# Performance work log

Hardware: AMD Instinct MI355X
Metric: run time of the kernel (lower is better)

The kernel has to match this reference:

```python
import jax, jax.numpy as jnp
import numpy as np

D_MODEL = 96
N_HEAD = 3
HEAD_DIM = D_MODEL // N_HEAD  # 32
D_FF = 2048
WIDTH = 65
HALF_W = (WIDTH - 1) // 2  # 32
EPS = 1e-5


def layer_norm(x, g, b):
    mu = jnp.mean(x, axis=-1, keepdims=True)
    var = jnp.mean(jnp.square(x - mu), axis=-1, keepdims=True)
    return (x - mu) * jax.lax.rsqrt(var + EPS) * g + b


def setup_inputs() -> dict:
    key = jax.random.key(0)
    ks = jax.random.split(key, 8)
    B, T = 8, 2048
    s = 0.05
    return {
        "x": jax.random.normal(ks[0], (B, D_MODEL, T), dtype=jnp.float32),
        "w_qkv": jax.random.normal(ks[1], (3 * D_MODEL, D_MODEL), dtype=jnp.float32) * s,
        "b_qkv": jnp.zeros((3 * D_MODEL,), dtype=jnp.float32),
        "w_out": jax.random.normal(ks[2], (D_MODEL, D_MODEL), dtype=jnp.float32) * s,
        "b_out": jnp.zeros((D_MODEL,), dtype=jnp.float32),
        "ln1_g": jnp.ones((D_MODEL,), dtype=jnp.float32),
        "ln1_b": jnp.zeros((D_MODEL,), dtype=jnp.float32),
        "w_ff1": jax.random.normal(ks[3], (D_FF, D_MODEL), dtype=jnp.float32) * s,
        "b_ff1": jnp.zeros((D_FF,), dtype=jnp.float32),
        "w_ff2": jax.random.normal(ks[4], (D_MODEL, D_FF), dtype=jnp.float32) * s,
        "b_ff2": jnp.zeros((D_MODEL,), dtype=jnp.float32),
        "ln2_g": jnp.ones((D_MODEL,), dtype=jnp.float32),
        "ln2_b": jnp.zeros((D_MODEL,), dtype=jnp.float32),
        "lnf_g": jnp.ones((D_MODEL,), dtype=jnp.float32),
        "lnf_b": jnp.zeros((D_MODEL,), dtype=jnp.float32),
    }


def reference(x, w_qkv, b_qkv, w_out, b_out, ln1_g, ln1_b, w_ff1, b_ff1,
              w_ff2, b_ff2, ln2_g, ln2_b, lnf_g, lnf_b):
    # x: (B, C, T) -> (B, T, C)
    h = jnp.transpose(x, (0, 2, 1))
    B, T, C = h.shape

    # --- multi-head self-attention with banded mask ---
    qkv = h @ w_qkv.T + b_qkv                      # (B, T, 3C)
    q, k, v = jnp.split(qkv, 3, axis=-1)
    q = q.reshape(B, T, N_HEAD, HEAD_DIM)
    k = k.reshape(B, T, N_HEAD, HEAD_DIM)
    v = v.reshape(B, T, N_HEAD, HEAD_DIM)

    scale = 1.0 / jnp.sqrt(jnp.float32(HEAD_DIM))
    scores = jnp.einsum("bthd,bshd->bhts", q, k) * scale  # (B, H, T, T)

    idx = jnp.arange(T)
    band = jnp.abs(idx[:, None] - idx[None, :]) <= HALF_W  # |i-j| <= half width
    scores = jnp.where(band[None, None], scores, jnp.float32(-jnp.inf))

    attn = jax.nn.softmax(scores, axis=-1)
    ctx = jnp.einsum("bhts,bshd->bthd", attn, v).reshape(B, T, C)
    attn_out = ctx @ w_out.T + b_out

    # --- post-norm encoder layer (dropout inactive / eval mode) ---
    h = layer_norm(h + attn_out, ln1_g, ln1_b)
    ff = jax.nn.relu(h @ w_ff1.T + b_ff1) @ w_ff2.T + b_ff2
    h = layer_norm(h + ff, ln2_g, ln2_b)

    # extra layernorm applied when width is not None
    h = layer_norm(h, lnf_g, lnf_b)

    # (B, T, C) -> (B, C, T)
    return jnp.transpose(h, (0, 2, 1))
```

## Files before the change

kernel.cpp:

```cpp
#include <hip/hip_runtime.h>
#include <hip/hip_bf16.h>

#define B 8
#define T 2048
#define C 96
#define NH 3
#define HD 32
#define FFD 2048
#define HALF_W 32
#define BT (B*T)

typedef __hip_bfloat16 bf16;
typedef __attribute__((ext_vector_type(8))) short short8;
typedef __attribute__((ext_vector_type(4))) short short4v;
typedef __attribute__((ext_vector_type(16))) float floatx16;

__device__ __forceinline__ short f2bs(float v){
    __hip_bfloat16 h = __float2bfloat16(v);
    return *reinterpret_cast<short*>(&h);
}
__device__ __forceinline__ float bs2f(short s){
    unsigned u = ((unsigned)(unsigned short)s) << 16;
    return __uint_as_float(u);
}
__device__ __forceinline__ int imin(int a, int b){ return a < b ? a : b; }
__device__ __forceinline__ int imax(int a, int b){ return a > b ? a : b; }
__device__ __forceinline__ short8 ld_b64x2(const short* p){
    short4v a = *(const short4v*)p;
    short4v b = *(const short4v*)(p + 4);
    short8 v;
    v[0]=a[0]; v[1]=a[1]; v[2]=a[2]; v[3]=a[3];
    v[4]=b[0]; v[5]=b[1]; v[6]=b[2]; v[7]=b[3];
    return v;
}
__device__ __forceinline__ int4 exch_pair(int a0,int a1,int b0,int b1,int hq){
    int ra0=__shfl_xor(a0,32), ra1=__shfl_xor(a1,32);
    int rb0=__shfl_xor(b0,32), rb1=__shfl_xor(b1,32);
    int4 s;
    s.x = hq ? rb0 : a0;
    s.y = hq ? rb1 : a1;
    s.z = hq ? b0  : ra0;
    s.w = hq ? b1  : ra1;
    return s;
}

__global__ void cvtw_kernel(const float* __restrict__ wq, const float* __restrict__ wo,
                            const float* __restrict__ w1, const float* __restrict__ w2,
                            bf16* __restrict__ dst){
    int i = blockIdx.x*256 + threadIdx.x;
    if(i < 27648){
        int e = i&7, lane = (i>>3)&63, r = i>>9;
        int ks = r%6, ot = r/6;
        int o = ot*32 + (lane&31);
        int k = ks*16 + (lane>>5)*8 + e;
        dst[i] = __float2bfloat16(wq[o*96 + k]);
    } else if(i < 36864){
        int j = i - 27648;
        int e = j&7, lane = (j>>3)&63, r = j>>9;
        int ks = r%6, ct = r/6;
        int c = ct*32 + (lane&31);
        int k = ks*16 + (lane>>5)*8 + e;
        dst[i] = __float2bfloat16(wo[c*96 + k]);
    } else if(i < 233472){
        int j = i - 36864;
        int e = j&7, lane = (j>>3)&63, r = j>>9;
        int ks = r%6; r /= 6;
        int w = r%4, jt = r/4;
        int row = jt*128 + w*32 + (lane&31);
        int k = ks*16 + (lane>>5)*8 + e;
        dst[i] = __float2bfloat16(w1[row*96 + k]);
    } else if(i < 430080){
        int j = i - 233472;
        int e = j&7, lane = (j>>3)&63, r = j>>9;
        int ct = r%3; r /= 3;
        int g = r%2; r /= 2;
        int w = r%4, jt = r/4;
        int c = ct*32 + (lane&31);
        int k = jt*128 + w*32 + g*16 + (lane>>5)*8 + e;
        dst[i] = __float2bfloat16(w2[c*FFD + k]);
    }
}

__global__ __launch_bounds__(256) void qkv_kernel(
    const float* __restrict__ x, const bf16* __restrict__ wqs,
    const float* __restrict__ bias, bf16* __restrict__ qswz,
    bf16* __restrict__ kswz, bf16* __restrict__ vbuf){
    __shared__ float xs[96*36];
    int b  = blockIdx.x >> 6;
    int tt = blockIdx.x & 63;
    int t0 = tt * 32;
    for(int e = threadIdx.x; e < 96*8; e += 256){
        int c = e >> 3, t4 = e & 7;
        *(float4*)(xs + c*36 + t4*4) =
            *(const float4*)(x + (size_t)b*C*T + (size_t)c*T + t0 + t4*4);
    }
    __syncthreads();
    const int w = threadIdx.x >> 6, lane = threadIdx.x & 63;
    const int lm = lane & 31, hq = lane >> 5;
    short8 bfr[6];
    #pragma unroll
    for(int ks = 0; ks < 6; ++ks){
        short8 v;
        #pragma unroll
        for(int i = 0; i < 8; ++i)
            v[i] = f2bs(xs[(ks*16 + hq*8 + i)*36 + lm]);
        bfr[ks] = v;
    }
    int nacc = (w == 0) ? 3 : 2;
    int ots[3] = {w, w+4, 8};
    floatx16 acc[3];
    #pragma unroll
    for(int i = 0; i < 3; ++i)
        #pragma unroll
        for(int r = 0; r < 16; ++r) acc[i][r] = 0.f;
    #pragma unroll
    for(int i = 0; i < 3; ++i){
        if(i < nacc){
            #pragma unroll
            for(int ks = 0; ks < 6; ++ks){
                short8 af = *(const short8*)((const short*)wqs
                              + (size_t)(ots[i]*6 + ks)*512 + lane*8);
                acc[i] = __builtin_amdgcn_mfma_f32_32x32x16_bf16(af, bfr[ks], acc[i], 0,0,0);
            }
        }
    }
    #pragma unroll
    for(int i = 0; i < 3; ++i){
        if(i < nacc){
            int ot = ots[i];
            int pkq[4][2];
            #pragma unroll
            for(int q = 0; q < 4; ++q){
                float4 bv = *(const float4*)(bias + ot*32 + 8*q + 4*hq);
                short4v t;
                t[0] = f2bs(acc[i][4*q+0] + bv.x);
                t[1] = f2bs(acc[i][4*q+1] + bv.y);
                t[2] = f2bs(acc[i][4*q+2] + bv.z);
                t[3] = f2bs(acc[i][4*q+3] + bv.w);
                int2 u = *(int2*)&t;
                pkq[q][0] = u.x; pkq[q][1] = u.y;
            }
            if(ot < 6){
                int type = ot/3, hh = ot%3;
                short* base = (short*)(type == 0 ? qswz : kswz)
                            + ((size_t)(b*NH + hh)*64 + tt)*1024 + lane*8;
                #pragma unroll
                for(int g = 0; g < 2; ++g){
                    int a0 = pkq[2*g][0],   a1 = pkq[2*g][1];
                    int b0 = pkq[2*g+1][0], b1v = pkq[2*g+1][1];
                    int ra0 = __shfl_xor(a0, 32),  ra1 = __shfl_xor(a1, 32);
                    int rb0 = __shfl_xor(b0, 32),  rb1 = __shfl_xor(b1v, 32);
                    int4 sfi;
                    sfi.x = hq ? rb0 : a0;
                    sfi.y = hq ? rb1 : a1;
                    sfi.z = hq ? b0  : ra0;
                    sfi.w = hq ? b1v : ra1;
                    *(int4*)(base + g*512) = sfi;
                }
            } else {
                int hh = ot - 6;
                short* rowp = (short*)vbuf + ((size_t)(b*NH + hh)*T + t0 + lm)*32;
                #pragma unroll
                for(int q = 0; q < 4; ++q){
                    int2 u; u.x = pkq[q][0]; u.y = pkq[q][1];
                    *(int2*)(rowp + 8*q + 4*hq) = u;
                }
            }
        }
    }
}

__global__ __launch_bounds__(192) void attn_op_kernel(
    const bf16* __restrict__ qswz, const bf16* __restrict__ kswz,
    const bf16* __restrict__ vbuf, const bf16* __restrict__ wos,
    const float* __restrict__ bias, const float* __restrict__ x,
    const float* __restrict__ g1, const float* __restrict__ bb1,
    bf16* __restrict__ h1b){
    __shared__ __align__(16) short VtS[3*3200];
    __shared__ __align__(16) short PtS[3][3200];
    __shared__ float LsS[3][32];
    __shared__ __align__(16) short ctxS[32*100];
    __shared__ float red1[2][3][32];
    const int tid = threadIdx.x;
    const int w = tid / 64, lane = tid & 63;
    const int lm = lane & 31, hq = lane >> 5;
    int b  = blockIdx.x >> 6;
    int tt = blockIdx.x & 63;
    int t0 = tt * 32;

    short8 wof[6];
    #pragma unroll
    for(int ks = 0; ks < 6; ++ks)
        wof[ks] = *(const short8*)((const short*)wos + (size_t)(w*6 + ks)*512 + lane*8);

    for(int e = tid; e < 576; e += 192){
        int hh = e / 192, rem = e % 192;
        int kp = rem >> 2, d8 = rem & 3;
        const short* vb = (const short*)vbuf + (size_t)(b*NH + hh)*T*32;
        int sa = imin(imax(t0 - 32 + 2*kp, 0), T-1);
        int sb = imin(imax(t0 - 32 + 2*kp + 1, 0), T-1);
        short8 va = *(const short8*)(vb + (size_t)sa*32 + d8*8);
        short8 v2 = *(const short8*)(vb + (size_t)sb*32 + d8*8);
        #pragma unroll
        for(int j = 0; j < 8; ++j){
            int val = (int)(unsigned short)va[j] | ((int)(unsigned short)v2[j] << 16);
            *(int*)(VtS + hh*3200 + (d8*8 + j)*100 + 2*kp) = val;
        }
    }
    const short* qsw = (const short*)qswz + ((size_t)(b*NH + w)*64 + tt)*1024 + lane*8;
    short8 qf0 = *(const short8*)(qsw);
    short8 qf1 = *(const short8*)(qsw + 512);
    floatx16 S[3];
    #pragma unroll
    for(int sub = 0; sub < 3; ++sub){
        int kt = imin(imax(tt - 1 + sub, 0), 63);
        const short* ksw = (const short*)kswz + ((size_t)(b*NH + w)*64 + kt)*1024 + lane*8;
        short8 kf0 = *(const short8*)(ksw);
        short8 kf1 = *(const short8*)(ksw + 512);
        floatx16 z;
        #pragma unroll
        for(int r = 0; r < 16; ++r) z[r] = 0.f;
        z = __builtin_amdgcn_mfma_f32_32x32x16_bf16(kf0, qf0, z, 0,0,0);
        z = __builtin_amdgcn_mfma_f32_32x32x16_bf16(kf1, qf1, z, 0,0,0);
        S[sub] = z;
    }
    const float scale = 0.17677669529663687f;
    float part = 0.f;
    #pragma unroll
    for(int sub = 0; sub < 3; ++sub){
        #pragma unroll
        for(int r = 0; r < 16; ++r){
            int key_local = sub*32 + (r&3) + 8*(r>>2) + 4*hq;
            int s_glob = t0 - 32 + key_local;
            int rel = key_local - lm;
            bool ok = (rel >= 0) && (rel <= 64) && (s_glob >= 0) && (s_glob < T);
            float p = ok ? __expf(S[sub][r]*scale) : 0.f;
            S[sub][r] = p;
            part += p;
        }
    }
    float ltot = part + __shfl_xor(part, 32);
    if(hq == 0) LsS[w][lm] = ltot;
    #pragma unroll
    for(int sub = 0; sub < 3; ++sub){
        #pragma unroll
        for(int q4 = 0; q4 < 4; ++q4){
            int kbase = sub*32 + 8*q4 + 4*hq;
            short4v pk;
            pk[0] = f2bs(S[sub][4*q4+0]);
            pk[1] = f2bs(S[sub][4*q4+1]);
            pk[2] = f2bs(S[sub][4*q4+2]);
            pk[3] = f2bs(S[sub][4*q4+3]);
            *(short4v*)(PtS[w] + lm*100 + kbase) = pk;
        }
    }
    __syncthreads();
    floatx16 O;
    #pragma unroll
    for(int r = 0; r < 16; ++r) O[r] = 0.f;
    #pragma unroll
    for(int ks = 0; ks < 6; ++ks){
        short8 pa = ld_b64x2(PtS[w] + lm*100 + ks*16 + hq*8);
        short8 vf = ld_b64x2(VtS + w*3200 + lm*100 + ks*16 + hq*8);
        O = __builtin_amdgcn_mfma_f32_32x32x16_bf16(pa, vf, O, 0,0,0);
    }
    #pragma unroll
    for(int r = 0; r < 16; ++r){
        int qr = (r&3) + 8*(r>>2) + 4*hq;
        float linv = 1.f / LsS[w][qr];
        ctxS[qr*100 + w*32 + lm] = f2bs(O[r]*linv);
    }
    __syncthreads();

    short8 bfr[6];
    #pragma unroll
    for(int ks = 0; ks < 6; ++ks)
        bfr[ks] = ld_b64x2(ctxS + lm*100 + ks*16 + hq*8);
    floatx16 acc;
    #pragma unroll
    for(int r = 0; r < 16; ++r) acc[r] = 0.f;
    #pragma unroll
    for(int ks = 0; ks < 6; ++ks)
        acc = __builtin_amdgcn_mfma_f32_32x32x16_bf16(wof[ks], bfr[ks], acc, 0,0,0);
    float vals[16];
    float p1 = 0.f, p2 = 0.f;
    #pragma unroll
    for(int q = 0; q < 4; ++q){
        int c = w*32 + 8*q + 4*hq;
        float4 bv = *(const float4*)(bias + c);
        float bva[4] = {bv.x, bv.y, bv.z, bv.w};
        #pragma unroll
        for(int r = 0; r < 4; ++r){
            float xv = x[(size_t)b*C*T + (size_t)(c + r)*T + t0 + lm];
            float v = acc[4*q+r] + bva[r] + xv;
            vals[4*q+r] = v;
            p1 += v; p2 += v*v;
        }
    }
    p1 += __shfl_xor(p1, 32);
    p2 += __shfl_xor(p2, 32);
    if(hq == 0){ red1[0][w][lm] = p1; red1[1][w][lm] = p2; }
    __syncthreads();
    float s  = red1[0][0][lm] + red1[0][1][lm] + red1[0][2][lm];
    float s2 = red1[1][0][lm] + red1[1][1][lm] + red1[1][2][lm];
    float mu = s * (1.0f/96.0f);
    float rstd = rsqrtf(s2*(1.0f/96.0f) - mu*mu + 1e-5f);
    int row = b*T + t0 + lm;
    #pragma unroll
    for(int q = 0; q < 4; ++q){
        int c = w*32 + 8*q + 4*hq;
        float4 gv = *(const float4*)(g1 + c);
        float4 bv = *(const float4*)(bb1 + c);
        float ga[4] = {gv.x, gv.y, gv.z, gv.w};
        float ba[4] = {bv.x, bv.y, bv.z, bv.w};
        short4v pk;
        #pragma unroll
        for(int r = 0; r < 4; ++r)
            pk[r] = f2bs((vals[4*q+r] - mu)*rstd*ga[r] + ba[r]);
        *(short4v*)((short*)h1b + (size_t)row*96 + c) = pk;
    }
}

__global__ __launch_bounds__(256, 2) void ff_kernel(
    const bf16* __restrict__ h1b,
    const bf16* __restrict__ w1s, const float* __restrict__ b1,
    const bf16* __restrict__ w2s, const float* __restrict__ b2,
    const float* __restrict__ g2, const float* __restrict__ bt2,
    const float* __restrict__ gf, const float* __restrict__ btf,
    float* __restrict__ out){
    __shared__ __align__(16) char smem[53760];
    float* REDP = (float*)smem;
    float* ZT   = (float*)smem;
    float* RED1 = (float*)(smem + 52224);
    float* RED2 = (float*)(smem + 52992);

    const int tid = threadIdx.x;
    const int w4 = tid >> 6, lane = tid & 63;
    const int lm = lane & 31, hq = lane >> 5;
    const int r0 = blockIdx.x * 32;
    const short* h1p = (const short*)h1b;

    short8 hf[6];
    #pragma unroll
    for(int ks = 0; ks < 6; ++ks)
        hf[ks] = *(const short8*)(h1p + (size_t)(r0 + lm)*96 + ks*16 + hq*8);

    floatx16 acc2[3];
    #pragma unroll
    for(int i = 0; i < 3; ++i)
        #pragma unroll
        for(int r = 0; r < 16; ++r) acc2[i][r] = 0.f;

    const short* w1b = (const short*)w1s + lane*8;
    const short* w2b = (const short*)w2s + lane*8;
    short8 cw1[6], cw2[6];
    #pragma unroll
    for(int ks = 0; ks < 6; ++ks)
        cw1[ks] = *(const short8*)(w1b + (size_t)(w4*6 + ks)*512);
    #pragma unroll
    for(int g = 0; g < 2; ++g)
        #pragma unroll
        for(int ct = 0; ct < 3; ++ct)
            cw2[g*3 + ct] = *(const short8*)(w2b + (size_t)((w4*2 + g)*3 + ct)*512);

    #pragma unroll
    for(int it = 0; it < 16; ++it){
        const int J  = w4 + it*4;
        const int Jn = (it < 15) ? J + 4 : w4;
        short8 nw1[6], nw2[6];
        #pragma unroll
        for(int ks = 0; ks < 6; ++ks)
            nw1[ks] = *(const short8*)(w1b + (size_t)(Jn*6 + ks)*512);
        #pragma unroll
        for(int g = 0; g < 2; ++g)
            #pragma unroll
            for(int ct = 0; ct < 3; ++ct)
                nw2[g*3 + ct] = *(const short8*)(w2b + (size_t)((Jn*2 + g)*3 + ct)*512);
        floatx16 a0;
        #pragma unroll
        for(int r = 0; r < 16; ++r) a0[r] = 0.f;
        #pragma unroll
        for(int ks = 0; ks < 6; ++ks)
            a0 = __builtin_amdgcn_mfma_f32_32x32x16_bf16(cw1[ks], hf[ks], a0, 0,0,0);
        int pk[4][2];
        #pragma unroll
        for(int q = 0; q < 4; ++q){
            float4 bv = *(const float4*)(b1 + J*32 + 8*q + 4*hq);
            float bva[4] = {bv.x, bv.y, bv.z, bv.w};
            short4v tv;
            #pragma unroll
            for(int r = 0; r < 4; ++r){
                float v0 = a0[4*q+r] + bva[r];
                tv[r] = f2bs(v0 > 0.f ? v0 : 0.f);
            }
            int2 uu = *(int2*)&tv; pk[q][0] = uu.x; pk[q][1] = uu.y;
        }
        #pragma unroll
        for(int g = 0; g < 2; ++g){
            int4 sfi = exch_pair(pk[2*g][0], pk[2*g][1], pk[2*g+1][0], pk[2*g+1][1], hq);
            short8 sf = *(short8*)&sfi;
            #pragma unroll
            for(int ct = 0; ct < 3; ++ct)
                acc2[ct] = __builtin_amdgcn_mfma_f32_32x32x16_bf16(cw2[g*3+ct], sf, acc2[ct], 0,0,0);
        }
        #pragma unroll
        for(int ks = 0; ks < 6; ++ks) cw1[ks] = nw1[ks];
        #pragma unroll
        for(int i = 0; i < 6; ++i) cw2[i] = nw2[i];
    }
    #pragma unroll
    for(int ct = 0; ct < 3; ++ct)
        #pragma unroll
        for(int q = 0; q < 4; ++q)
            #pragma unroll
            for(int r = 0; r < 4; ++r)
                REDP[(w4*3 + ct)*1088 + lane*17 + 4*q + r] = acc2[ct][4*q+r];
    __syncthreads();

    float fv[16];
    float e1 = 0.f, e2 = 0.f;
    if(w4 < 3){
        #pragma unroll
        for(int q = 0; q < 4; ++q){
            int cb = w4*32 + 8*q + 4*hq;
            float4 bv = *(const float4*)(b2 + cb);
            float bva[4] = {bv.x, bv.y, bv.z, bv.w};
            short4v hv = *(const short4v*)(h1p + (size_t)(r0 + lm)*96 + cb);
            #pragma unroll
            for(int r = 0; r < 4; ++r){
                float v = REDP[(0*3 + w4)*1088 + lane*17 + 4*q + r]
                        + REDP[(1*3 + w4)*1088 + lane*17 + 4*q + r]
                        + REDP[(2*3 + w4)*1088 + lane*17 + 4*q + r]
                        + REDP[(3*3 + w4)*1088 + lane*17 + 4*q + r]
                        + bva[r] + bs2f(hv[r]);
                fv[4*q+r] = v;
                e1 += v; e2 += v*v;
            }
        }
        e1 += __shfl_xor(e1, 32);
        e2 += __shfl_xor(e2, 32);
        if(hq == 0){ RED1[w4*32 + lm] = e1; RED1[96 + w4*32 + lm] = e2; }
    }
    __syncthreads();
    float f1 = 0.f, f2 = 0.f;
    if(w4 < 3){
        float s  = RED1[lm] + RED1[32 + lm] + RED1[64 + lm];
        float s2 = RED1[96 + lm] + RED1[128 + lm] + RED1[160 + lm];
        float mu = s * (1.0f/96.0f);
        float rstd = rsqrtf(s2*(1.0f/96.0f) - mu*mu + 1e-5f);
        #pragma unroll
        for(int q = 0; q < 4; ++q){
            int c = w4*32 + 8*q + 4*hq;
            float4 gv = *(const float4*)(g2 + c);
            float4 bv = *(const float4*)(bt2 + c);
            float ga[4] = {gv.x, gv.y, gv.z, gv.w};
            float ba[4] = {bv.x, bv.y, bv.z, bv.w};
            #pragma unroll
            for(int r = 0; r < 4; ++r){
                float y = (fv[4*q+r] - mu)*rstd*ga[r] + ba[r];
                fv[4*q+r] = y;
                f1 += y; f2 += y*y;
            }
        }
        f1 += __shfl_xor(f1, 32);
        f2 += __shfl_xor(f2, 32);
        if(hq == 0){ RED2[w4*32 + lm] = f1; RED2[96 + w4*32 + lm] = f2; }
    }
    __syncthreads();
    if(w4 < 3){
        float s  = RED2[lm] + RED2[32 + lm] + RED2[64 + lm];
        float s2 = RED2[96 + lm] + RED2[128 + lm] + RED2[160 + lm];
        float mu = s * (1.0f/96.0f);
        float rstd = rsqrtf(s2*(1.0f/96.0f) - mu*mu + 1e-5f);
        #pragma unroll
        for(int q = 0; q < 4; ++q){
            int c = w4*32 + 8*q + 4*hq;
            float4 gv = *(const float4*)(gf + c);
            float4 bv = *(const float4*)(btf + c);
            float ga[4] = {gv.x, gv.y, gv.z, gv.w};
            float ba[4] = {bv.x, bv.y, bv.z, bv.w};
            #pragma unroll
            for(int r = 0; r < 4; ++r)
                ZT[(c + r)*36 + lm] = (fv[4*q+r] - mu)*rstd*ga[r] + ba[r];
        }
    }
    __syncthreads();
    const int bb = r0 / T, t0g = r0 % T;
    float* ob = out + (size_t)bb*C*T + t0g;
    for(int e = tid; e < 96*8; e += 256){
        int c = e >> 3, qq = e & 7;
        *(float4*)(ob + (size_t)c*T + qq*4) = *(const float4*)(ZT + c*36 + qq*4);
    }
}

extern "C" void kernel_launch(void* const* d_in, const int* in_sizes, int n_in,
                              void* d_out, int out_size, void* d_ws, size_t ws_size,
                              hipStream_t stream) {
    const float* x     = (const float*)d_in[0];
    const float* w_qkv = (const float*)d_in[1];
    const float* b_qkv = (const float*)d_in[2];
    const float* w_out = (const float*)d_in[3];
    const float* b_out = (const float*)d_in[4];
    const float* ln1_g = (const float*)d_in[5];
    const float* ln1_b = (const float*)d_in[6];
    const float* w_ff1 = (const float*)d_in[7];
    const float* b_ff1 = (const float*)d_in[8];
    const float* w_ff2 = (const float*)d_in[9];
    const float* b_ff2 = (const float*)d_in[10];
    const float* ln2_g = (const float*)d_in[11];
    const float* ln2_b = (const float*)d_in[12];
    const float* lnf_g = (const float*)d_in[13];
    const float* lnf_b = (const float*)d_in[14];
    float* out = (float*)d_out;

    char* wsb = (char*)d_ws;
    bf16*  qswz  = (bf16*)wsb;
    bf16*  kswz  = (bf16*)(wsb + 3145728);
    bf16*  vbuf  = (bf16*)(wsb + 6291456);
    bf16*  h1b   = (bf16*)(wsb + 9437184);
    bf16*  wts   = (bf16*)(wsb + 12582912);
    bf16*  wqs   = wts;
    bf16*  wos   = wts + 27648;
    bf16*  w1s   = wts + 36864;
    bf16*  w2s   = wts + 233472;

    cvtw_kernel   <<<1680, 256, 0, stream>>>(w_qkv, w_out, w_ff1, w_ff2, wts);
    qkv_kernel    <<<BT/32, 256, 0, stream>>>(x, wqs, b_qkv, qswz, kswz, vbuf);
    attn_op_kernel<<<B*(T/32), 192, 0, stream>>>(qswz, kswz, vbuf, wos, b_out, x,
                                                 ln1_g, ln1_b, h1b);
    ff_kernel     <<<BT/32, 256, 0, stream>>>(h1b, w1s, b_ff1, w2s, b_ff2,
                                              ln2_g, ln2_b, lnf_g, lnf_b, out);
}
```

Before: 126.5 us.

## Process 64 rows per FF block to reuse weight fragments across two M-tiles

```diff
diff --git a/kernel.cpp b/kernel.cpp
--- a/kernel.cpp
+++ b/kernel.cpp
@@ -328,168 +328,200 @@
     const float* __restrict__ g2, const float* __restrict__ bt2,
     const float* __restrict__ gf, const float* __restrict__ btf,
     float* __restrict__ out){
-    __shared__ __align__(16) char smem[53760];
+    __shared__ __align__(16) char smem[55296];
     float* REDP = (float*)smem;
     float* ZT   = (float*)smem;
     float* RED1 = (float*)(smem + 52224);
-    float* RED2 = (float*)(smem + 52992);
+    float* RED2 = (float*)(smem + 53760);
 
     const int tid = threadIdx.x;
     const int w4 = tid >> 6, lane = tid & 63;
     const int lm = lane & 31, hq = lane >> 5;
-    const int r0 = blockIdx.x * 32;
+    const int r0 = blockIdx.x * 64;
     const short* h1p = (const short*)h1b;
 
-    short8 hf[6];
-    #pragma unroll
-    for(int ks = 0; ks < 6; ++ks)
-        hf[ks] = *(const short8*)(h1p + (size_t)(r0 + lm)*96 + ks*16 + hq*8);
-
-    floatx16 acc2[3];
-    #pragma unroll
-    for(int i = 0; i < 3; ++i)
-        #pragma unroll
-        for(int r = 0; r < 16; ++r) acc2[i][r] = 0.f;
+    short8 hf[2][6];
+    #pragma unroll
+    for(int mt = 0; mt < 2; ++mt)
+        #pragma unroll
+        for(int ks = 0; ks < 6; ++ks)
+            hf[mt][ks] = *(const short8*)(h1p + (size_t)(r0 + mt*32 + lm)*96 + ks*16 + hq*8);
+
+    floatx16 acc2[2][3];
+    #pragma unroll
+    for(int mt = 0; mt < 2; ++mt)
+        #pragma unroll
+        for(int i = 0; i < 3; ++i)
+            #pragma unroll
+            for(int r = 0; r < 16; ++r) acc2[mt][i][r] = 0.f;
 
     const short* w1b = (const short*)w1s + lane*8;
     const short* w2b = (const short*)w2s + lane*8;
-    short8 cw1[6], cw2[6];
+    short8 cw1[6];
     #pragma unroll
     for(int ks = 0; ks < 6; ++ks)
         cw1[ks] = *(const short8*)(w1b + (size_t)(w4*6 + ks)*512);
-    #pragma unroll
-    for(int g = 0; g < 2; ++g)
-        #pragma unroll
-        for(int ct = 0; ct < 3; ++ct)
-            cw2[g*3 + ct] = *(const short8*)(w2b + (size_t)((w4*2 + g)*3 + ct)*512);
-
-    #pragma unroll
+
     for(int it = 0; it < 16; ++it){
         const int J  = w4 + it*4;
         const int Jn = (it < 15) ? J + 4 : w4;
-        short8 nw1[6], nw2[6];
+        short8 w2f[6];
+        #pragma unroll
+        for(int g = 0; g < 2; ++g)
+            #pragma unroll
+            for(int ct = 0; ct < 3; ++ct)
+                w2f[g*3 + ct] = *(const short8*)(w2b + (size_t)((J*2 + g)*3 + ct)*512);
+        short8 nw1[6];
         #pragma unroll
         for(int ks = 0; ks < 6; ++ks)
             nw1[ks] = *(const short8*)(w1b + (size_t)(Jn*6 + ks)*512);
-        #pragma unroll
-        for(int g = 0; g < 2; ++g)
-            #pragma unroll
-            for(int ct = 0; ct < 3; ++ct)
-                nw2[g*3 + ct] = *(const short8*)(w2b + (size_t)((Jn*2 + g)*3 + ct)*512);
-        floatx16 a0;
-        #pragma unroll
-        for(int r = 0; r < 16; ++r) a0[r] = 0.f;
-        #pragma unroll
-        for(int ks = 0; ks < 6; ++ks)
-            a0 = __builtin_amdgcn_mfma_f32_32x32x16_bf16(cw1[ks], hf[ks], a0, 0,0,0);
-        int pk[4][2];
+        floatx16 a0, a1;
+        #pragma unroll
+        for(int r = 0; r < 16; ++r){ a0[r] = 0.f; a1[r] = 0.f; }
+        #pragma unroll
+        for(int ks = 0; ks < 6; ++ks){
+            a0 = __builtin_amdgcn_mfma_f32_32x32x16_bf16(cw1[ks], hf[0][ks], a0, 0,0,0);
+            a1 = __builtin_amdgcn_mfma_f32_32x32x16_bf16(cw1[ks], hf[1][ks], a1, 0,0,0);
+        }
+        int pk[2][4][2];
         #pragma unroll
         for(int q = 0; q < 4; ++q){
             float4 bv = *(const float4*)(b1 + J*32 + 8*q + 4*hq);
             float bva[4] = {bv.x, bv.y, bv.z, bv.w};
-            short4v tv;
+            short4v t0v, t1v;
             #pragma unroll
             for(int r = 0; r < 4; ++r){
                 float v0 = a0[4*q+r] + bva[r];
-                tv[r] = f2bs(v0 > 0.f ? v0 : 0.f);
-            }
-            int2 uu = *(int2*)&tv; pk[q][0] = uu.x; pk[q][1] = uu.y;
+                float v1 = a1[4*q+r] + bva[r];
+                t0v[r] = f2bs(v0 > 0.f ? v0 : 0.f);
+                t1v[r] = f2bs(v1 > 0.f ? v1 : 0.f);
+            }
+            int2 u0 = *(int2*)&t0v; int2 u1 = *(int2*)&t1v;
+            pk[0][q][0] = u0.x; pk[0][q][1] = u0.y;
+            pk[1][q][0] = u1.x; pk[1][q][1] = u1.y;
         }
         #pragma unroll
         for(int g = 0; g < 2; ++g){
-            int4 sfi = exch_pair(pk[2*g][0], pk[2*g][1], pk[2*g+1][0], pk[2*g+1][1], hq);
-            short8 sf = *(short8*)&sfi;
-            #pragma unroll
-            for(int ct = 0; ct < 3; ++ct)
-                acc2[ct] = __builtin_amdgcn_mfma_f32_32x32x16_bf16(cw2[g*3+ct], sf, acc2[ct], 0,0,0);
+            #pragma unroll
+            for(int mt = 0; mt < 2; ++mt){
+                int4 sfi = exch_pair(pk[mt][2*g][0], pk[mt][2*g][1],
+                                     pk[mt][2*g+1][0], pk[mt][2*g+1][1], hq);
+                short8 sf = *(short8*)&sfi;
+                #pragma unroll
+                for(int ct = 0; ct < 3; ++ct)
+                    acc2[mt][ct] = __builtin_amdgcn_mfma_f32_32x32x16_bf16(
+                                       w2f[g*3+ct], sf, acc2[mt][ct], 0,0,0);
+            }
         }
         #pragma unroll
         for(int ks = 0; ks < 6; ++ks) cw1[ks] = nw1[ks];
-        #pragma unroll
-        for(int i = 0; i < 6; ++i) cw2[i] = nw2[i];
-    }
-    #pragma unroll
-    for(int ct = 0; ct < 3; ++ct)
-        #pragma unroll
-        for(int q = 0; q < 4; ++q)
-            #pragma unroll
-            for(int r = 0; r < 4; ++r)
-                REDP[(w4*3 + ct)*1088 + lane*17 + 4*q + r] = acc2[ct][4*q+r];
-    __syncthreads();
-
-    float fv[16];
-    float e1 = 0.f, e2 = 0.f;
+    }
+
+    float fv[2][16];
+    float e1m[2], e2m[2];
+    #pragma unroll
+    for(int mt = 0; mt < 2; ++mt){
+        #pragma unroll
+        for(int ct = 0; ct < 3; ++ct)
+            #pragma unroll
+            for(int q = 0; q < 4; ++q)
+                #pragma unroll
+                for(int r = 0; r < 4; ++r)
+                    REDP[(w4*3 + ct)*1088 + lane*17 + 4*q + r] = acc2[mt][ct][4*q+r];
+        __syncthreads();
+        if(w4 < 3){
+            float e1 = 0.f, e2 = 0.f;
+            #pragma unroll
+            for(int q = 0; q < 4; ++q){
+                int cb = w4*32 + 8*q + 4*hq;
+                float4 bv = *(const float4*)(b2 + cb);
+                float bva[4] = {bv.x, bv.y, bv.z, bv.w};
+                short4v hv = *(const short4v*)(h1p + (size_t)(r0 + mt*32 + lm)*96 + cb);
+                #pragma unroll
+                for(int r = 0; r < 4; ++r){
+                    float v = REDP[(0*3 + w4)*1088 + lane*17 + 4*q + r]
+                            + REDP[(1*3 + w4)*1088 + lane*17 + 4*q + r]
+                            + REDP[(2*3 + w4)*1088 + lane*17 + 4*q + r]
+                            + REDP[(3*3 + w4)*1088 + lane*17 + 4*q + r]
+                            + bva[r] + bs2f(hv[r]);
+                    fv[mt][4*q+r] = v;
+                    e1 += v; e2 += v*v;
+                }
+            }
+            e1m[mt] = e1 + __shfl_xor(e1, 32);
+            e2m[mt] = e2 + __shfl_xor(e2, 32);
+        }
+        __syncthreads();
+    }
+    if(w4 < 3 && hq == 0){
+        #pragma unroll
+        for(int mt = 0; mt < 2; ++mt){
+            RED1[mt*192 + w4*32 + lm] = e1m[mt];
+            RED1[mt*192 + 96 + w4*32 + lm] = e2m[mt];
+        }
+    }
+    __syncthreads();
+    float f1m[2], f2m[2];
     if(w4 < 3){
         #pragma unroll
-        for(int q = 0; q < 4; ++q){
-            int cb = w4*32 + 8*q + 4*hq;
-            float4 bv = *(const float4*)(b2 + cb);
-            float bva[4] = {bv.x, bv.y, bv.z, bv.w};
-            short4v hv = *(const short4v*)(h1p + (size_t)(r0 + lm)*96 + cb);
-            #pragma unroll
-            for(int r = 0; r < 4; ++r){
-                float v = REDP[(0*3 + w4)*1088 + lane*17 + 4*q + r]
-                        + REDP[(1*3 + w4)*1088 + lane*17 + 4*q + r]
-                        + REDP[(2*3 + w4)*1088 + lane*17 + 4*q + r]
-                        + REDP[(3*3 + w4)*1088 + lane*17 + 4*q + r]
-                        + bva[r] + bs2f(hv[r]);
-                fv[4*q+r] = v;
-                e1 += v; e2 += v*v;
-            }
-        }
-        e1 += __shfl_xor(e1, 32);
-        e2 += __shfl_xor(e2, 32);
-        if(hq == 0){ RED1[w4*32 + lm] = e1; RED1[96 + w4*32 + lm] = e2; }
-    }
-    __syncthreads();
-    float f1 = 0.f, f2 = 0.f;
+        for(int mt = 0; mt < 2; ++mt){
+            float s  = RED1[mt*192 + lm] + RED1[mt*192 + 32 + lm] + RED1[mt*192 + 64 + lm];
+            float s2 = RED1[mt*192 + 96 + lm] + RED1[mt*192 + 128 + lm] + RED1[mt*192 + 160 + lm];
+            float mu = s * (1.0f/96.0f);
+            float rstd = rsqrtf(s2*(1.0f/96.0f) - mu*mu + 1e-5f);
+            float f1 = 0.f, f2 = 0.f;
+            #pragma unroll
+            for(int q = 0; q < 4; ++q){
+                int c = w4*32 + 8*q + 4*hq;
+                float4 gv = *(const float4*)(g2 + c);
+                float4 bv = *(const float4*)(bt2 + c);
+                float ga[4] = {gv.x, gv.y, gv.z, gv.w};
+                float ba[4] = {bv.x, bv.y, bv.z, bv.w};
+                #pragma unroll
+                for(int r = 0; r < 4; ++r){
+                    float y = (fv[mt][4*q+r] - mu)*rstd*ga[r] + ba[r];
+                    fv[mt][4*q+r] = y;
+                    f1 += y; f2 += y*y;
+                }
+            }
+            f1m[mt] = f1 + __shfl_xor(f1, 32);
+            f2m[mt] = f2 + __shfl_xor(f2, 32);
+        }
+        if(hq == 0){
+            #pragma unroll
+            for(int mt = 0; mt < 2; ++mt){
+                RED2[mt*192 + w4*32 + lm] = f1m[mt];
+                RED2[mt*192 + 96 + w4*32 + lm] = f2m[mt];
+            }
+        }
+    }
+    __syncthreads();
     if(w4 < 3){
-        float s  = RED1[lm] + RED1[32 + lm] + RED1[64 + lm];
-        float s2 = RED1[96 + lm] + RED1[128 + lm] + RED1[160 + lm];
-        float mu = s * (1.0f/96.0f);
-        float rstd = rsqrtf(s2*(1.0f/96.0f) - mu*mu + 1e-5f);
-        #pragma unroll
-        for(int q = 0; q < 4; ++q){
-            int c = w4*32 + 8*q + 4*hq;
-            float4 gv = *(const float4*)(g2 + c);
-            float4 bv = *(const float4*)(bt2 + c);
-            float ga[4] = {gv.x, gv.y, gv.z, gv.w};
-            float ba[4] = {bv.x, bv.y, bv.z, bv.w};
-            #pragma unroll
-            for(int r = 0; r < 4; ++r){
-                float y = (fv[4*q+r] - mu)*rstd*ga[r] + ba[r];
-                fv[4*q+r] = y;
-                f1 += y; f2 += y*y;
-            }
-        }
-        f1 += __shfl_xor(f1, 32);
-        f2 += __shfl_xor(f2, 32);
-        if(hq == 0){ RED2[w4*32 + lm] = f1; RED2[96 + w4*32 + lm] = f2; }
-    }
-    __syncthreads();
-    if(w4 < 3){
-        float s  = RED2[lm] + RED2[32 + lm] + RED2[64 + lm];
-        float s2 = RED2[96 + lm] + RED2[128 + lm] + RED2[160 + lm];
-        float mu = s * (1.0f/96.0f);
-        float rstd = rsqrtf(s2*(1.0f/96.0f) - mu*mu + 1e-5f);
-        #pragma unroll
-        for(int q = 0; q < 4; ++q){
-            int c = w4*32 + 8*q + 4*hq;
-            float4 gv = *(const float4*)(gf + c);
-            float4 bv = *(const float4*)(btf + c);
-            float ga[4] = {gv.x, gv.y, gv.z, gv.w};
-            float ba[4] = {bv.x, bv.y, bv.z, bv.w};
-            #pragma unroll
-            for(int r = 0; r < 4; ++r)
-                ZT[(c + r)*36 + lm] = (fv[4*q+r] - mu)*rstd*ga[r] + ba[r];
+        #pragma unroll
+        for(int mt = 0; mt < 2; ++mt){
+            float s  = RED2[mt*192 + lm] + RED2[mt*192 + 32 + lm] + RED2[mt*192 + 64 + lm];
+            float s2 = RED2[mt*192 + 96 + lm] + RED2[mt*192 + 128 + lm] + RED2[mt*192 + 160 + lm];
+            float mu = s * (1.0f/96.0f);
+            float rstd = rsqrtf(s2*(1.0f/96.0f) - mu*mu + 1e-5f);
+            #pragma unroll
+            for(int q = 0; q < 4; ++q){
+                int c = w4*32 + 8*q + 4*hq;
+                float4 gv = *(const float4*)(gf + c);
+                float4 bv = *(const float4*)(btf + c);
+                float ga[4] = {gv.x, gv.y, gv.z, gv.w};
+                float ba[4] = {bv.x, bv.y, bv.z, bv.w};
+                #pragma unroll
+                for(int r = 0; r < 4; ++r)
+                    ZT[(c + r)*68 + mt*32 + lm] = (fv[mt][4*q+r] - mu)*rstd*ga[r] + ba[r];
+            }
         }
     }
     __syncthreads();
     const int bb = r0 / T, t0g = r0 % T;
     float* ob = out + (size_t)bb*C*T + t0g;
-    for(int e = tid; e < 96*8; e += 256){
-        int c = e >> 3, qq = e & 7;
-        *(float4*)(ob + (size_t)c*T + qq*4) = *(const float4*)(ZT + c*36 + qq*4);
+    for(int e = tid; e < 96*16; e += 256){
+        int c = e >> 4, tg = e & 15;
+        *(float4*)(ob + (size_t)c*T + tg*4) = *(const float4*)(ZT + c*68 + tg*4);
     }
 }
 
@@ -528,6 +560,6 @@
     qkv_kernel    <<<BT/32, 256, 0, stream>>>(x, wqs, b_qkv, qswz, kswz, vbuf);
     attn_op_kernel<<<B*(T/32), 192, 0, stream>>>(qswz, kswz, vbuf, wos, b_out, x,
                                                  ln1_g, ln1_b, h1b);
-    ff_kernel     <<<BT/32, 256, 0, stream>>>(h1b, w1s, b_ff1, w2s, b_ff2,
+    ff_kernel     <<<BT/64, 256, 0, stream>>>(h1b, w1s, b_ff1, w2s, b_ff2,
                                               ln2_g, ln2_b, lnf_g, lnf_b, out);
 }
```

New measurement: 126.5 us. Within noise of the previous version (+0.0%).
